# Kernel optimization log

Measured on AMD Instinct MI355X. Metric: run time of the kernel, lower is better.

The kernel has to match this reference:

```python
import jax, jax.numpy as jnp
import numpy as np

N, C, T, V = 32, 256, 256, 25
CI = C // 2
BN_EPS = 1e-5


def setup_inputs() -> dict:
    key = jax.random.key(0)
    ks = jax.random.split(key, 11)
    s = 1.0 / np.sqrt(C)
    si = 1.0 / np.sqrt(CI)
    return {
        "x": jax.random.normal(ks[0], (N, C, T, V), dtype=jnp.float32),
        "Wg": jax.random.normal(ks[1], (CI, C), dtype=jnp.float32) * s,
        "bg": jax.random.normal(ks[2], (CI,), dtype=jnp.float32) * s,
        "Wth": jax.random.normal(ks[3], (CI, C), dtype=jnp.float32) * s,
        "bth": jax.random.normal(ks[4], (CI,), dtype=jnp.float32) * s,
        "Wph": jax.random.normal(ks[5], (CI, C), dtype=jnp.float32) * s,
        "bph": jax.random.normal(ks[6], (CI,), dtype=jnp.float32) * s,
        "Ww": jax.random.normal(ks[7], (C, CI), dtype=jnp.float32) * si,
        "bw": jax.random.normal(ks[8], (C,), dtype=jnp.float32) * si,
        "gamma": jax.random.normal(ks[9], (C,), dtype=jnp.float32) * 0.1,
        "beta": jax.random.normal(ks[10], (C,), dtype=jnp.float32) * 0.1,
    }


def reference(x, Wg, bg, Wth, bth, Wph, bph, Ww, bw, gamma, beta):
    n, c, t, v = x.shape
    ci = Wg.shape[0]
    # [N,C,T,V] -> [N*V, C, T] (permute(0,3,1,2).reshape)
    xf = jnp.transpose(x, (0, 3, 1, 2)).reshape(n * v, c, t)
    # 1x1 Conv1d == channel GEMM
    g_x = jnp.einsum('bct,oc->bot', xf, Wg) + bg[:, None]      # [N*V, Ci, T]
    g_x = g_x.reshape(n, v * ci, t).transpose(0, 2, 1)         # [N, T, V*Ci]
    xmean = xf.reshape(n, v, c, t).mean(axis=1)                # [N, C, T]
    theta = (jnp.einsum('nct,oc->not', xmean, Wth) + bth[:, None]).transpose(0, 2, 1)  # [N,T,Ci]
    phi = jnp.einsum('nct,oc->not', xmean, Wph) + bph[:, None]  # [N, Ci, T]
    f = jnp.matmul(theta, phi)                                  # [N, T, T]
    f = jax.nn.softmax(f, axis=-1)
    y = jnp.matmul(f, g_x)                                      # [N, T, V*Ci]
    y = y.transpose(0, 2, 1).reshape(n * v, ci, t)              # [N*V, Ci, T]
    wy = jnp.einsum('bct,oc->bot', y, Ww) + bw[:, None]         # [N*V, C, T]
    # BatchNorm1d (training mode: batch stats over (batch, T))
    mu = wy.mean(axis=(0, 2))
    var = wy.var(axis=(0, 2))
    wy = (wy - mu[:, None]) * jax.lax.rsqrt(var[:, None] + BN_EPS) * gamma[:, None] + beta[:, None]
    z = wy + xf                                                 # residual
    return jnp.transpose(z.reshape(n, v, c, t), (0, 2, 3, 1))   # [N, C, T, V]
```

## Files before the change

kernel.cpp:

```cpp
#include <hip/hip_runtime.h>

typedef unsigned short u16;
using s8v = __attribute__((ext_vector_type(8))) short;
using f4v = __attribute__((ext_vector_type(4))) float;

constexpr int kN = 32, kC = 256, kT = 256, kV = 25, kCI = 128;
constexpr int kTV = kT * kV;
constexpr int kCIV = kCI * kV;
constexpr int kSAMP = kN * kT * kV;
constexpr int SYY_B = 256;

__device__ __forceinline__ float bf2f(u16 v) {
  return __uint_as_float(((unsigned)v) << 16);
}
__device__ __forceinline__ u16 f2bf(float f) {
  unsigned u = __float_as_uint(f);
  return (u16)((u + 0x7FFFu + ((u >> 16) & 1u)) >> 16);
}

__global__ __launch_bounds__(256) void k_prep(const float* __restrict__ x, u16* __restrict__ x_bf,
                                              float* __restrict__ xm) {
  __shared__ float sm[6400];
  size_t base = (size_t)blockIdx.x * 6400;
  const float4* src = (const float4*)(x + base);
  ushort4* dst = (ushort4*)(x_bf + base);
  for (int i = threadIdx.x; i < 1600; i += 256) {
    float4 v = src[i];
    ((float4*)sm)[i] = v;
    ushort4 b;
    b.x = f2bf(v.x); b.y = f2bf(v.y); b.z = f2bf(v.z); b.w = f2bf(v.w);
    dst[i] = b;
  }
  __syncthreads();
  const float* r = sm + threadIdx.x * 25;
  float s = 0.f;
#pragma unroll
  for (int j = 0; j < 25; ++j) s += r[j];
  xm[(size_t)blockIdx.x * 256 + threadIdx.x] = s * (1.0f / kV);
}

__global__ __launch_bounds__(256) void k_thetaphi(
    const float* __restrict__ xmean, const float* __restrict__ Wth, const float* __restrict__ bth,
    const float* __restrict__ Wph, const float* __restrict__ bph,
    u16* __restrict__ thT, u16* __restrict__ phT) {
  int n = blockIdx.x >> 5;
  int o0 = (blockIdx.x & 31) * 4;
  int t = threadIdx.x;
  __shared__ float wt[4][kC], wp[4][kC];
  for (int i = threadIdx.x; i < 1024; i += 256) {
    wt[i >> 8][i & 255] = Wth[(o0 + (i >> 8)) * kC + (i & 255)];
    wp[i >> 8][i & 255] = Wph[(o0 + (i >> 8)) * kC + (i & 255)];
  }
  __syncthreads();
  const float* xmp = xmean + (size_t)n * kC * kT + t;
  float a[4], p[4];
#pragma unroll
  for (int j = 0; j < 4; ++j) { a[j] = bth[o0 + j]; p[j] = bph[o0 + j]; }
#pragma unroll 4
  for (int c = 0; c < kC; ++c) {
    float xv = xmp[c * kT];
#pragma unroll
    for (int j = 0; j < 4; ++j) {
      a[j] = fmaf(wt[j][c], xv, a[j]);
      p[j] = fmaf(wp[j][c], xv, p[j]);
    }
  }
  size_t rowb = ((size_t)n * kT + t) * kCI + o0;
#pragma unroll
  for (int j = 0; j < 4; ++j) {
    thT[rowb + j] = f2bf(a[j]);
    phT[rowb + j] = f2bf(p[j]);
  }
}

__global__ __launch_bounds__(512) void k_fmfma(const u16* __restrict__ thT, const u16* __restrict__ phT,
                                               u16* __restrict__ f) {
  const int n = blockIdx.x >> 1;
  const int tc0 = (blockIdx.x & 1) * 128;
  const int tid = threadIdx.x, lane = tid & 63, w = tid >> 6;
  const int wM = w & 3, wr = wM * 64, wc = (w >> 2) * 64;
  const int l15 = lane & 15, l4 = lane >> 4;
  __shared__ float redm[4][128], reds[4][128];
  f4v acc[4][4];
#pragma unroll
  for (int i = 0; i < 4; ++i)
#pragma unroll
    for (int j = 0; j < 4; ++j) acc[i][j] = f4v{0.f, 0.f, 0.f, 0.f};
#pragma unroll
  for (int ks = 0; ks < 4; ++ks) {
    s8v af[4], bf[4];
#pragma unroll
    for (int fi = 0; fi < 4; ++fi)
      af[fi] = *(const s8v*)(phT + ((size_t)(n * 256 + wr + fi * 16 + l15) * kCI + ks * 32 + l4 * 8));
#pragma unroll
    for (int g = 0; g < 4; ++g)
      bf[g] = *(const s8v*)(thT + ((size_t)(n * 256 + tc0 + wc + g * 16 + l15) * kCI + ks * 32 + l4 * 8));
#pragma unroll
    for (int g = 0; g < 4; ++g)
#pragma unroll
      for (int fi = 0; fi < 4; ++fi)
        acc[fi][g] = __builtin_amdgcn_mfma_f32_16x16x32_bf16(af[fi], bf[g], acc[fi][g], 0, 0, 0);
  }
  float mx[4], sm[4];
#pragma unroll
  for (int g = 0; g < 4; ++g) {
    float m = -1e30f;
#pragma unroll
    for (int fi = 0; fi < 4; ++fi)
#pragma unroll
      for (int r = 0; r < 4; ++r) m = fmaxf(m, acc[fi][g][r]);
    m = fmaxf(m, __shfl_xor(m, 16));
    m = fmaxf(m, __shfl_xor(m, 32));
    mx[g] = m;
  }
  if (l4 == 0)
#pragma unroll
    for (int g = 0; g < 4; ++g) redm[wM][wc + g * 16 + l15] = mx[g];
  __syncthreads();
#pragma unroll
  for (int g = 0; g < 4; ++g) {
    int col = wc + g * 16 + l15;
    mx[g] = fmaxf(fmaxf(redm[0][col], redm[1][col]), fmaxf(redm[2][col], redm[3][col]));
  }
#pragma unroll
  for (int g = 0; g < 4; ++g) {
    float s = 0.f;
#pragma unroll
    for (int fi = 0; fi < 4; ++fi)
#pragma unroll
      for (int r = 0; r < 4; ++r) {
        float e = __expf(acc[fi][g][r] - mx[g]);
        acc[fi][g][r] = e;
        s += e;
      }
    s += __shfl_xor(s, 16);
    s += __shfl_xor(s, 32);
    sm[g] = s;
  }
  if (l4 == 0)
#pragma unroll
    for (int g = 0; g < 4; ++g) reds[wM][wc + g * 16 + l15] = sm[g];
  __syncthreads();
#pragma unroll
  for (int g = 0; g < 4; ++g) {
    int col = wc + g * 16 + l15;
    float inv = 1.0f / (reds[0][col] + reds[1][col] + reds[2][col] + reds[3][col]);
    int t = tc0 + col;
#pragma unroll
    for (int fi = 0; fi < 4; ++fi) {
      int tp0 = wr + fi * 16 + l4 * 4;
      ushort4 st;
      st.x = f2bf(acc[fi][g][0] * inv);
      st.y = f2bf(acc[fi][g][1] * inv);
      st.z = f2bf(acc[fi][g][2] * inv);
      st.w = f2bf(acc[fi][g][3] * inv);
      *(ushort4*)(f + (size_t)(n * 256 + t) * 256 + tp0) = st;
    }
  }
}

__global__ __launch_bounds__(256) void k_cvtW(const float* __restrict__ Wg, const float* __restrict__ Ww,
                                              u16* __restrict__ Wg_fl, u16* __restrict__ Ww_fl) {
  int i = blockIdx.x * 256 + threadIdx.x;
  { int m = i >> 8, k = i & 255; Wg_fl[(size_t)((k >> 3) * 128 + m) * 8 + (k & 7)] = f2bf(Wg[i]); }
  { int m = i >> 7, k = i & 127; Ww_fl[(size_t)((k >> 3) * 256 + m) * 8 + (k & 7)] = f2bf(Ww[i]); }
}

template <int K_TOT, int NCOLS, int MODE>
__global__ __launch_bounds__(256) void k_gemm(
    const u16* __restrict__ A_, const u16* __restrict__ B_, const float* __restrict__ bias,
    void* __restrict__ outp, const float* __restrict__ scale, const float* __restrict__ shift,
    const u16* __restrict__ xres) {
  constexpr int KSTEPS = K_TOT / 32;
  constexpr int M_TOT = (MODE == 0) ? 128 : 256;
  __shared__ uint4 Bs[512];
  const int n = blockIdx.z, m0 = blockIdx.y * 128, n0 = blockIdx.x * 128;
  const int tid = threadIdx.x, lane = tid & 63, w = tid >> 6;
  const int wr = (w >> 1) * 64, wc = (w & 1) * 64;
  const int l15 = lane & 15, l4 = lane >> 4;
  const u16* Bn = B_ + (size_t)n * K_TOT * NCOLS + n0;
  const int scol = tid & 127, sk0 = tid >> 7;
  f4v acc[4][4];
#pragma unroll
  for (int i = 0; i < 4; ++i)
#pragma unroll
    for (int j = 0; j < 4; ++j) acc[i][j] = f4v{0.f, 0.f, 0.f, 0.f};

  for (int ks = 0; ks < KSTEPS; ++ks) {
    __syncthreads();
#pragma unroll
    for (int p = 0; p < 2; ++p) {
      int ksub = sk0 + p * 2;
      const u16* src = Bn + (size_t)(ks * 32 + ksub * 8) * NCOLS + scol;
      union { u16 u[8]; uint4 v; } pk;
#pragma unroll
      for (int j = 0; j < 8; ++j) pk.u[j] = src[(size_t)j * NCOLS];
      int blk = ksub * 128 + scol;
      blk ^= (blk >> 2) & 3;
      Bs[blk] = pk.v;
    }
    __syncthreads();
    s8v af[4];
#pragma unroll
    for (int fi = 0; fi < 4; ++fi) {
      int m = m0 + wr + fi * 16 + l15;
      const u16* ap;
      if constexpr (MODE == 1)
        ap = A_ + ((size_t)(n * 256 + m) * 256 + ks * 32 + l4 * 8);
      else
        ap = A_ + (size_t)((ks * 4 + l4) * M_TOT + m) * 8;
      af[fi] = *(const s8v*)ap;
    }
#pragma unroll
    for (int g = 0; g < 4; ++g) {
      int blk = l4 * 128 + wc + g * 16 + l15;
      blk ^= (blk >> 2) & 3;
      s8v bf = *(const s8v*)&Bs[blk];
#pragma unroll
      for (int fi = 0; fi < 4; ++fi)
        acc[fi][g] = __builtin_amdgcn_mfma_f32_16x16x32_bf16(af[fi], bf, acc[fi][g], 0, 0, 0);
    }
  }
#pragma unroll
  for (int fi = 0; fi < 4; ++fi) {
    int growb = m0 + wr + fi * 16 + l4 * 4;
#pragma unroll
    for (int g = 0; g < 4; ++g) {
      int gcol = n0 + wc + g * 16 + l15;
#pragma unroll
      for (int r = 0; r < 4; ++r) {
        int grow = growb + r;
        float vv = acc[fi][g][r];
        if constexpr (MODE == 0) {
          vv += bias[grow];
          int t = gcol / 25, v5 = gcol - t * 25;
          ((u16*)outp)[((size_t)n * kT + t) * kCIV + grow * 25 + v5] = f2bf(vv);
        } else if constexpr (MODE == 1) {
          int ci = gcol / 25, v5 = gcol - ci * 25;
          ((u16*)outp)[((size_t)n * kCI + ci) * kTV + grow * 25 + v5] = f2bf(vv);
        } else {
          size_t idx = ((size_t)n * kC + grow) * kTV + gcol;
          ((float*)outp)[idx] = vv * scale[grow] + shift[grow] + bf2f(xres[idx]);
        }
      }
    }
  }
}

__global__ __launch_bounds__(256) void k_syy(const u16* __restrict__ yb, float* __restrict__ psyy,
                                             float* __restrict__ psy) {
  const int b = blockIdx.x, n = b >> 3, kc = b & 7;
  const int kbase = kc * 800;
  const int tid = threadIdx.x, lane = tid & 63, w = tid >> 6;
  const int wr = (w >> 1) * 64, wc = (w & 1) * 64, l15 = lane & 15, l4 = lane >> 4;
  const u16* Y = yb + (size_t)n * kCI * kTV;
  f4v acc[4][4];
#pragma unroll
  for (int i = 0; i < 4; ++i)
#pragma unroll
    for (int j = 0; j < 4; ++j) acc[i][j] = f4v{0.f, 0.f, 0.f, 0.f};
  float syl[4] = {0.f, 0.f, 0.f, 0.f};
  for (int ks = 0; ks < 25; ++ks) {
    int k = kbase + ks * 32 + l4 * 8;
    s8v af[4], bf[4];
#pragma unroll
    for (int fi = 0; fi < 4; ++fi) {
      af[fi] = *(const s8v*)(Y + (size_t)(wr + fi * 16 + l15) * kTV + k);
      bf[fi] = *(const s8v*)(Y + (size_t)(wc + fi * 16 + l15) * kTV + k);
    }
#pragma unroll
    for (int fi = 0; fi < 4; ++fi)
#pragma unroll
      for (int j = 0; j < 8; ++j) syl[fi] += bf2f((u16)af[fi][j]);
#pragma unroll
    for (int g = 0; g < 4; ++g)
#pragma unroll
      for (int fi = 0; fi < 4; ++fi)
        acc[fi][g] = __builtin_amdgcn_mfma_f32_16x16x32_bf16(af[fi], bf[g], acc[fi][g], 0, 0, 0);
  }
  float* pb = psyy + (size_t)b * 16384;
#pragma unroll
  for (int fi = 0; fi < 4; ++fi)
#pragma unroll
    for (int g = 0; g < 4; ++g)
#pragma unroll
      for (int r = 0; r < 4; ++r)
        pb[(wr + fi * 16 + l4 * 4 + r) * kCI + wc + g * 16 + l15] = acc[fi][g][r];
#pragma unroll
  for (int fi = 0; fi < 4; ++fi) {
    float s = syl[fi];
    s += __shfl_xor(s, 16);
    s += __shfl_xor(s, 32);
    if ((w & 1) == 0 && l4 == 0) psy[b * kCI + wr + fi * 16 + l15] = s;
  }
}

__global__ __launch_bounds__(256) void k_reduce(const float* __restrict__ psyy, const float* __restrict__ psy,
                                                float* __restrict__ syy, float* __restrict__ sy) {
  if (blockIdx.x < 64) {
    int i = blockIdx.x * 256 + threadIdx.x;
    float s = 0.f;
    for (int b = 0; b < SYY_B; ++b) s += psyy[(size_t)b * 16384 + i];
    syy[i] = s;
  } else if (threadIdx.x < kCI) {
    float s = 0.f;
    for (int b = 0; b < SYY_B; ++b) s += psy[b * kCI + threadIdx.x];
    sy[threadIdx.x] = s;
  }
}

__global__ __launch_bounds__(128) void k_stats(const float* __restrict__ syy, const float* __restrict__ sy,
                                               const float* __restrict__ Ww, const float* __restrict__ bw,
                                               const float* __restrict__ gamma, const float* __restrict__ beta,
                                               float* __restrict__ scale, float* __restrict__ shift) {
  int c2 = blockIdx.x;
  int tid = threadIdx.x;
  __shared__ float wsm[kCI];
  __shared__ float red1[kCI], red2[kCI];
  wsm[tid] = Ww[c2 * kCI + tid];
  __syncthreads();
  float val = 0.f;
#pragma unroll 8
  for (int ci = 0; ci < kCI; ++ci) val = fmaf(wsm[ci], syy[ci * kCI + tid], val);
  red1[tid] = wsm[tid] * sy[tid];
  red2[tid] = val * wsm[tid];
  __syncthreads();
  for (int s = 64; s > 0; s >>= 1) {
    if (tid < s) { red1[tid] += red1[tid + s]; red2[tid] += red2[tid + s]; }
    __syncthreads();
  }
  if (tid == 0) {
    const float invS = 1.0f / (float)kSAMP;
    float m1 = red1[0] * invS;
    float b = bw[c2];
    float mu = m1 + b;
    float e2 = red2[0] * invS + 2.f * b * m1 + b * b;
    float var = e2 - mu * mu;
    float rstd = rsqrtf(var + 1e-5f);
    float sc = rstd * gamma[c2];
    scale[c2] = sc;
    shift[c2] = beta[c2] + (b - mu) * sc;
  }
}

extern "C" void kernel_launch(void* const* d_in, const int* in_sizes, int n_in,
                              void* d_out, int out_size, void* d_ws, size_t ws_size,
                              hipStream_t stream) {
  const float* x     = (const float*)d_in[0];
  const float* Wg    = (const float*)d_in[1];
  const float* bg    = (const float*)d_in[2];
  const float* Wth   = (const float*)d_in[3];
  const float* bth   = (const float*)d_in[4];
  const float* Wph   = (const float*)d_in[5];
  const float* bph   = (const float*)d_in[6];
  const float* Ww    = (const float*)d_in[7];
  const float* bw    = (const float*)d_in[8];
  const float* gamma = (const float*)d_in[9];
  const float* beta  = (const float*)d_in[10];
  float* out = (float*)d_out;

  char* wsb = (char*)d_ws;
  float* xmean = (float*)(wsb);
  u16*   thT   = (u16*)(wsb + (8u << 20));
  u16*   phT   = (u16*)(wsb + (10u << 20));
  u16*   f_bf  = (u16*)(wsb + (12u << 20));
  float* psy   = (float*)(wsb + (16u << 20));
  float* syy   = (float*)(wsb + (17u << 20));
  float* sy    = syy + 16384;
  float* scale = sy + 128;
  float* shift = scale + 256;
  u16* Wg_fl = (u16*)(wsb + (18u << 20));
  u16* Ww_fl = Wg_fl + 32768;
  u16* x_bf  = (u16*)(wsb + (19u << 20));
  u16* g2    = (u16*)(wsb + (119u << 20));
  float* psyy = (float*)(wsb + (119u << 20));
  u16* yb    = (u16*)(wsb + (172u << 20));

  k_prep<<<8192, 256, 0, stream>>>(x, x_bf, xmean);
  k_cvtW<<<128, 256, 0, stream>>>(Wg, Ww, Wg_fl, Ww_fl);
  k_thetaphi<<<1024, 256, 0, stream>>>(xmean, Wth, bth, Wph, bph, thT, phT);
  k_fmfma<<<64, 512, 0, stream>>>(thT, phT, f_bf);
  k_gemm<256, kTV, 0><<<dim3(50, 1, 32), 256, 0, stream>>>(
      Wg_fl, x_bf, bg, (void*)g2, nullptr, nullptr, nullptr);
  k_gemm<256, kCIV, 1><<<dim3(25, 2, 32), 256, 0, stream>>>(
      f_bf, g2, nullptr, (void*)yb, nullptr, nullptr, nullptr);
  k_syy<<<SYY_B, 256, 0, stream>>>(yb, psyy, psy);
  k_reduce<<<65, 256, 0, stream>>>(psyy, psy, syy, sy);
  k_stats<<<256, 128, 0, stream>>>(syy, sy, Ww, bw, gamma, beta, scale, shift);
  k_gemm<128, kTV, 2><<<dim3(50, 2, 32), 256, 0, stream>>>(
      Ww_fl, yb, nullptr, (void*)out, scale, shift, x_bf);
}
```

Measured before the change: 363.5 us.

## Store GEMM operands in k-packed fragment layout and drop LDS staging

Producers (k_prep, k_fmfma, the g and y GEMM epilogues) now write their bf16 outputs in a layout that packs 8 consecutive k values per column. This lets k_gemm load A and B MFMA fragments directly from global memory as 16-byte vectors, removing the strided scalar gathers, LDS staging and barriers. The y GEMM writes both a row-major copy for the stats kernel and a packed copy for the final GEMM. The residual now reads the fp32 input x directly instead of a bf16 copy. The cost is extra write traffic and possible cache pressure from relying on global memory for fragment reuse.

Result: slower. 450.2 us (+23.9%).

```diff
diff --git a/kernel.cpp b/kernel.cpp
--- a/kernel.cpp
+++ b/kernel.cpp
@@ -6,7 +6,6 @@
 
 constexpr int kN = 32, kC = 256, kT = 256, kV = 25, kCI = 128;
 constexpr int kTV = kT * kV;
-constexpr int kCIV = kCI * kV;
 constexpr int kSAMP = kN * kT * kV;
 constexpr int SYY_B = 256;
 
@@ -18,25 +17,36 @@
   return (u16)((u + 0x7FFFu + ((u >> 16) & 1u)) >> 16);
 }
 
-__global__ __launch_bounds__(256) void k_prep(const float* __restrict__ x, u16* __restrict__ x_bf,
+__global__ __launch_bounds__(256) void k_prep(const float* __restrict__ x, u16* __restrict__ x_fl,
                                               float* __restrict__ xm) {
-  __shared__ float sm[6400];
-  size_t base = (size_t)blockIdx.x * 6400;
-  const float4* src = (const float4*)(x + base);
-  ushort4* dst = (ushort4*)(x_bf + base);
-  for (int i = threadIdx.x; i < 1600; i += 256) {
-    float4 v = src[i];
-    ((float4*)sm)[i] = v;
-    ushort4 b;
-    b.x = f2bf(v.x); b.y = f2bf(v.y); b.z = f2bf(v.z); b.w = f2bf(v.w);
-    dst[i] = b;
-  }
-  __syncthreads();
-  const float* r = sm + threadIdx.x * 25;
-  float s = 0.f;
-#pragma unroll
-  for (int j = 0; j < 25; ++j) s += r[j];
-  xm[(size_t)blockIdx.x * 256 + threadIdx.x] = s * (1.0f / kV);
+  __shared__ float sm[8][1600];
+  const int n = blockIdx.x >> 5, cg = blockIdx.x & 31;
+  const int tid = threadIdx.x;
+  u16* xfn = x_fl + (size_t)n * (kC / 8) * kTV * 8;
+  for (int chunk = 0; chunk < 4; ++chunk) {
+    const int col0 = chunk * 1600;
+    for (int e = tid; e < 3200; e += 256) {
+      int r = e / 400, c4 = e % 400;
+      float4 v = *(const float4*)(x + ((size_t)(n * kC + cg * 8 + r) * kTV + col0) + c4 * 4);
+      *(float4*)&sm[r][c4 * 4] = v;
+    }
+    __syncthreads();
+    for (int col = tid; col < 1600; col += 256) {
+      union { u16 u[8]; uint4 v; } pk;
+#pragma unroll
+      for (int r = 0; r < 8; ++r) pk.u[r] = f2bf(sm[r][col]);
+      *(uint4*)(xfn + (size_t)(cg * kTV + col0 + col) * 8) = pk.v;
+    }
+    for (int i = tid; i < 512; i += 256) {
+      int c = i >> 6, tl = i & 63;
+      float s = 0.f;
+      const float* p = &sm[c][tl * 25];
+#pragma unroll
+      for (int j = 0; j < 25; ++j) s += p[j];
+      xm[(size_t)(n * kC + cg * 8 + c) * kT + chunk * 64 + tl] = s * (1.0f / kV);
+    }
+    __syncthreads();
+  }
 }
 
 __global__ __launch_bounds__(256) void k_thetaphi(
@@ -74,7 +84,7 @@
 }
 
 __global__ __launch_bounds__(512) void k_fmfma(const u16* __restrict__ thT, const u16* __restrict__ phT,
-                                               u16* __restrict__ f) {
+                                               u16* __restrict__ f_fl) {
   const int n = blockIdx.x >> 1;
   const int tc0 = (blockIdx.x & 1) * 128;
   const int tid = threadIdx.x, lane = tid & 63, w = tid >> 6;
@@ -154,7 +164,7 @@
       st.y = f2bf(acc[fi][g][1] * inv);
       st.z = f2bf(acc[fi][g][2] * inv);
       st.w = f2bf(acc[fi][g][3] * inv);
-      *(ushort4*)(f + (size_t)(n * 256 + t) * 256 + tp0) = st;
+      *(ushort4*)(f_fl + (size_t)n * 65536 + (size_t)((tp0 >> 3) * 256 + t) * 8 + (tp0 & 7)) = st;
     }
   }
 }
@@ -169,57 +179,37 @@
 template <int K_TOT, int NCOLS, int MODE>
 __global__ __launch_bounds__(256) void k_gemm(
     const u16* __restrict__ A_, const u16* __restrict__ B_, const float* __restrict__ bias,
-    void* __restrict__ outp, const float* __restrict__ scale, const float* __restrict__ shift,
-    const u16* __restrict__ xres) {
+    void* __restrict__ outp, void* __restrict__ outp2, const float* __restrict__ scale,
+    const float* __restrict__ shift, const float* __restrict__ xres) {
   constexpr int KSTEPS = K_TOT / 32;
   constexpr int M_TOT = (MODE == 0) ? 128 : 256;
-  __shared__ uint4 Bs[512];
   const int n = blockIdx.z, m0 = blockIdx.y * 128, n0 = blockIdx.x * 128;
   const int tid = threadIdx.x, lane = tid & 63, w = tid >> 6;
   const int wr = (w >> 1) * 64, wc = (w & 1) * 64;
   const int l15 = lane & 15, l4 = lane >> 4;
-  const u16* Bn = B_ + (size_t)n * K_TOT * NCOLS + n0;
-  const int scol = tid & 127, sk0 = tid >> 7;
+  const u16* Bn = B_ + (size_t)n * (K_TOT / 8) * NCOLS * 8;
+  const u16* An = (MODE == 1) ? A_ + (size_t)n * 65536 : A_;
   f4v acc[4][4];
 #pragma unroll
   for (int i = 0; i < 4; ++i)
 #pragma unroll
     for (int j = 0; j < 4; ++j) acc[i][j] = f4v{0.f, 0.f, 0.f, 0.f};
 
+#pragma unroll 2
   for (int ks = 0; ks < KSTEPS; ++ks) {
-    __syncthreads();
-#pragma unroll
-    for (int p = 0; p < 2; ++p) {
-      int ksub = sk0 + p * 2;
-      const u16* src = Bn + (size_t)(ks * 32 + ksub * 8) * NCOLS + scol;
-      union { u16 u[8]; uint4 v; } pk;
-#pragma unroll
-      for (int j = 0; j < 8; ++j) pk.u[j] = src[(size_t)j * NCOLS];
-      int blk = ksub * 128 + scol;
-      blk ^= (blk >> 2) & 3;
-      Bs[blk] = pk.v;
-    }
-    __syncthreads();
-    s8v af[4];
-#pragma unroll
-    for (int fi = 0; fi < 4; ++fi) {
-      int m = m0 + wr + fi * 16 + l15;
-      const u16* ap;
-      if constexpr (MODE == 1)
-        ap = A_ + ((size_t)(n * 256 + m) * 256 + ks * 32 + l4 * 8);
-      else
-        ap = A_ + (size_t)((ks * 4 + l4) * M_TOT + m) * 8;
-      af[fi] = *(const s8v*)ap;
-    }
-#pragma unroll
-    for (int g = 0; g < 4; ++g) {
-      int blk = l4 * 128 + wc + g * 16 + l15;
-      blk ^= (blk >> 2) & 3;
-      s8v bf = *(const s8v*)&Bs[blk];
+    const int ksub = ks * 4 + l4;
+    s8v af[4], bf[4];
+#pragma unroll
+    for (int fi = 0; fi < 4; ++fi)
+      af[fi] = *(const s8v*)(An + (size_t)(ksub * M_TOT + m0 + wr + fi * 16 + l15) * 8);
+#pragma unroll
+    for (int g = 0; g < 4; ++g)
+      bf[g] = *(const s8v*)(Bn + (size_t)(ksub * NCOLS + n0 + wc + g * 16 + l15) * 8);
+#pragma unroll
+    for (int g = 0; g < 4; ++g)
 #pragma unroll
       for (int fi = 0; fi < 4; ++fi)
-        acc[fi][g] = __builtin_amdgcn_mfma_f32_16x16x32_bf16(af[fi], bf, acc[fi][g], 0, 0, 0);
-    }
+        acc[fi][g] = __builtin_amdgcn_mfma_f32_16x16x32_bf16(af[fi], bf[g], acc[fi][g], 0, 0, 0);
   }
 #pragma unroll
   for (int fi = 0; fi < 4; ++fi) {
@@ -234,13 +224,15 @@
         if constexpr (MODE == 0) {
           vv += bias[grow];
           int t = gcol / 25, v5 = gcol - t * 25;
-          ((u16*)outp)[((size_t)n * kT + t) * kCIV + grow * 25 + v5] = f2bf(vv);
+          ((u16*)outp)[(size_t)n * 819200 + (size_t)((t >> 3) * 3200 + grow * 25 + v5) * 8 + (t & 7)] = f2bf(vv);
         } else if constexpr (MODE == 1) {
           int ci = gcol / 25, v5 = gcol - ci * 25;
-          ((u16*)outp)[((size_t)n * kCI + ci) * kTV + grow * 25 + v5] = f2bf(vv);
+          u16 b = f2bf(vv);
+          ((u16*)outp)[((size_t)n * kCI + ci) * kTV + grow * 25 + v5] = b;
+          ((u16*)outp2)[(size_t)n * 819200 + (size_t)((ci >> 3) * 6400 + grow * 25 + v5) * 8 + (ci & 7)] = b;
         } else {
           size_t idx = ((size_t)n * kC + grow) * kTV + gcol;
-          ((float*)outp)[idx] = vv * scale[grow] + shift[grow] + bf2f(xres[idx]);
+          ((float*)outp)[idx] = vv * scale[grow] + shift[grow] + xres[idx];
         }
       }
     }
@@ -363,7 +355,7 @@
   float* xmean = (float*)(wsb);
   u16*   thT   = (u16*)(wsb + (8u << 20));
   u16*   phT   = (u16*)(wsb + (10u << 20));
-  u16*   f_bf  = (u16*)(wsb + (12u << 20));
+  u16*   f_fl  = (u16*)(wsb + (12u << 20));
   float* psy   = (float*)(wsb + (16u << 20));
   float* syy   = (float*)(wsb + (17u << 20));
   float* sy    = syy + 16384;
@@ -371,22 +363,23 @@
   float* shift = scale + 256;
   u16* Wg_fl = (u16*)(wsb + (18u << 20));
   u16* Ww_fl = Wg_fl + 32768;
-  u16* x_bf  = (u16*)(wsb + (19u << 20));
-  u16* g2    = (u16*)(wsb + (119u << 20));
+  u16* x_fl  = (u16*)(wsb + (19u << 20));
+  u16* yb_fl = x_fl;
+  u16* g2_fl = (u16*)(wsb + (119u << 20));
   float* psyy = (float*)(wsb + (119u << 20));
-  u16* yb    = (u16*)(wsb + (172u << 20));
-
-  k_prep<<<8192, 256, 0, stream>>>(x, x_bf, xmean);
+  u16* yb_rm = (u16*)(wsb + (169u << 20));
+
+  k_prep<<<1024, 256, 0, stream>>>(x, x_fl, xmean);
   k_cvtW<<<128, 256, 0, stream>>>(Wg, Ww, Wg_fl, Ww_fl);
   k_thetaphi<<<1024, 256, 0, stream>>>(xmean, Wth, bth, Wph, bph, thT, phT);
-  k_fmfma<<<64, 512, 0, stream>>>(thT, phT, f_bf);
+  k_fmfma<<<64, 512, 0, stream>>>(thT, phT, f_fl);
   k_gemm<256, kTV, 0><<<dim3(50, 1, 32), 256, 0, stream>>>(
-      Wg_fl, x_bf, bg, (void*)g2, nullptr, nullptr, nullptr);
-  k_gemm<256, kCIV, 1><<<dim3(25, 2, 32), 256, 0, stream>>>(
-      f_bf, g2, nullptr, (void*)yb, nullptr, nullptr, nullptr);
-  k_syy<<<SYY_B, 256, 0, stream>>>(yb, psyy, psy);
+      Wg_fl, x_fl, bg, (void*)g2_fl, nullptr, nullptr, nullptr, nullptr);
+  k_gemm<256, 3200, 1><<<dim3(25, 2, 32), 256, 0, stream>>>(
+      f_fl, g2_fl, nullptr, (void*)yb_rm, (void*)yb_fl, nullptr, nullptr, nullptr);
+  k_syy<<<SYY_B, 256, 0, stream>>>(yb_rm, psyy, psy);
   k_reduce<<<65, 256, 0, stream>>>(psyy, psy, syy, sy);
   k_stats<<<256, 128, 0, stream>>>(syy, sy, Ww, bw, gamma, beta, scale, shift);
   k_gemm<128, kTV, 2><<<dim3(50, 2, 32), 256, 0, stream>>>(
-      Ww_fl, yb, nullptr, (void*)out, scale, shift, x_bf);
-}
+      Ww_fl, yb_fl, nullptr, (void*)out, nullptr, scale, shift, x);
+}
```

## Fuse theta/phi projection into attention kernel using MFMA on bf16 weights

Applied to the files above, without the earlier changes.

Removes the scalar FP32 theta/phi projection kernel and instead computes theta and phi inside the attention kernel with bf16 MFMA, staging xmean as bf16 in LDS and keeping the projected values in LDS for the T×T score GEMM and softmax. Wth and Wph are converted to a fragment-friendly bf16 layout in the weight conversion kernel. This drops one launch and the global round trip of theta/phi. In exchange, each of the 64 blocks recomputes phi for all 256 time steps, xmean is now rounded to bf16 before the projection, and the fused kernel uses large LDS with only 64 blocks running.

New measurement: 354.0 us. 2.6% less time.

```diff
diff --git a/kernel.cpp b/kernel.cpp
--- a/kernel.cpp
+++ b/kernel.cpp
@@ -39,68 +39,111 @@
   xm[(size_t)blockIdx.x * 256 + threadIdx.x] = s * (1.0f / kV);
 }
 
-__global__ __launch_bounds__(256) void k_thetaphi(
-    const float* __restrict__ xmean, const float* __restrict__ Wth, const float* __restrict__ bth,
-    const float* __restrict__ Wph, const float* __restrict__ bph,
-    u16* __restrict__ thT, u16* __restrict__ phT) {
-  int n = blockIdx.x >> 5;
-  int o0 = (blockIdx.x & 31) * 4;
-  int t = threadIdx.x;
-  __shared__ float wt[4][kC], wp[4][kC];
-  for (int i = threadIdx.x; i < 1024; i += 256) {
-    wt[i >> 8][i & 255] = Wth[(o0 + (i >> 8)) * kC + (i & 255)];
-    wp[i >> 8][i & 255] = Wph[(o0 + (i >> 8)) * kC + (i & 255)];
-  }
-  __syncthreads();
-  const float* xmp = xmean + (size_t)n * kC * kT + t;
-  float a[4], p[4];
-#pragma unroll
-  for (int j = 0; j < 4; ++j) { a[j] = bth[o0 + j]; p[j] = bph[o0 + j]; }
-#pragma unroll 4
-  for (int c = 0; c < kC; ++c) {
-    float xv = xmp[c * kT];
-#pragma unroll
-    for (int j = 0; j < 4; ++j) {
-      a[j] = fmaf(wt[j][c], xv, a[j]);
-      p[j] = fmaf(wp[j][c], xv, p[j]);
-    }
-  }
-  size_t rowb = ((size_t)n * kT + t) * kCI + o0;
-#pragma unroll
-  for (int j = 0; j < 4; ++j) {
-    thT[rowb + j] = f2bf(a[j]);
-    phT[rowb + j] = f2bf(p[j]);
-  }
-}
-
-__global__ __launch_bounds__(512) void k_fmfma(const u16* __restrict__ thT, const u16* __restrict__ phT,
+__global__ __launch_bounds__(256) void k_cvtW(const float* __restrict__ Wg, const float* __restrict__ Ww,
+                                              const float* __restrict__ Wth, const float* __restrict__ Wph,
+                                              u16* __restrict__ Wg_fl, u16* __restrict__ Ww_fl,
+                                              u16* __restrict__ Wthph_fl) {
+  int i = blockIdx.x * 256 + threadIdx.x;
+  { int m = i >> 8, k = i & 255; Wg_fl[(size_t)((k >> 3) * 128 + m) * 8 + (k & 7)] = f2bf(Wg[i]); }
+  { int m = i >> 7, k = i & 127; Ww_fl[(size_t)((k >> 3) * 256 + m) * 8 + (k & 7)] = f2bf(Ww[i]); }
+  { int m = i >> 8, k = i & 255;
+    Wthph_fl[(size_t)((k >> 3) * 256 + m) * 8 + (k & 7)] = f2bf(Wth[i]);
+    Wthph_fl[(size_t)((k >> 3) * 256 + (m + 128)) * 8 + (k & 7)] = f2bf(Wph[i]); }
+}
+
+__global__ __launch_bounds__(512) void k_fattn(const float* __restrict__ xmean,
+                                               const u16* __restrict__ Wthph_fl,
+                                               const float* __restrict__ bth, const float* __restrict__ bph,
                                                u16* __restrict__ f) {
-  const int n = blockIdx.x >> 1;
-  const int tc0 = (blockIdx.x & 1) * 128;
+  __shared__ __align__(16) u16 lds[49152];
+  const int n = blockIdx.x >> 1, tc0 = (blockIdx.x & 1) * 128;
   const int tid = threadIdx.x, lane = tid & 63, w = tid >> 6;
-  const int wM = w & 3, wr = wM * 64, wc = (w >> 2) * 64;
   const int l15 = lane & 15, l4 = lane >> 4;
-  __shared__ float redm[4][128], reds[4][128];
-  f4v acc[4][4];
+  const int wro = (w & 3) * 64, wct = (w >> 2) * 128;
+  f4v acc[4][8];
 #pragma unroll
   for (int i = 0; i < 4; ++i)
 #pragma unroll
-    for (int j = 0; j < 4; ++j) acc[i][j] = f4v{0.f, 0.f, 0.f, 0.f};
+    for (int j = 0; j < 8; ++j) acc[i][j] = f4v{0.f, 0.f, 0.f, 0.f};
+  for (int ch = 0; ch < 2; ++ch) {
+    __syncthreads();
+    for (int e = tid; e < 8192; e += 512) {
+      int cc = e >> 6, t4 = (e & 63) * 4;
+      float4 v = *(const float4*)(xmean + (((size_t)(n * 256 + ch * 128 + cc)) << 8) + t4);
+      u16* d = &lds[(((cc >> 3) * 256 + t4) << 3) + (cc & 7)];
+      d[0] = f2bf(v.x); d[8] = f2bf(v.y); d[16] = f2bf(v.z); d[24] = f2bf(v.w);
+    }
+    __syncthreads();
+#pragma unroll
+    for (int ks = 0; ks < 4; ++ks) {
+      const int ksub = ks * 4 + l4;
+      s8v af[4], bf[8];
+#pragma unroll
+      for (int fi = 0; fi < 4; ++fi)
+        af[fi] = *(const s8v*)(Wthph_fl + (size_t)((ch * 16 + ksub) * 256 + wro + fi * 16 + l15) * 8);
+#pragma unroll
+      for (int g = 0; g < 8; ++g)
+        bf[g] = *(const s8v*)&lds[((ksub * 256 + wct + g * 16 + l15) << 3)];
+#pragma unroll
+      for (int g = 0; g < 8; ++g)
+#pragma unroll
+        for (int fi = 0; fi < 4; ++fi)
+          acc[fi][g] = __builtin_amdgcn_mfma_f32_16x16x32_bf16(af[fi], bf[g], acc[fi][g], 0, 0, 0);
+    }
+  }
+  __syncthreads();
+#pragma unroll
+  for (int fi = 0; fi < 4; ++fi) {
+    int o0 = wro + fi * 16 + l4 * 4;
+    bool isTh = o0 < 128;
+    float bb[4];
+#pragma unroll
+    for (int r = 0; r < 4; ++r) bb[r] = isTh ? bth[o0 + r] : bph[o0 - 128 + r];
+#pragma unroll
+    for (int g = 0; g < 8; ++g) {
+      int t = wct + g * 16 + l15;
+      ushort4 pk;
+      pk.x = f2bf(acc[fi][g][0] + bb[0]);
+      pk.y = f2bf(acc[fi][g][1] + bb[1]);
+      pk.z = f2bf(acc[fi][g][2] + bb[2]);
+      pk.w = f2bf(acc[fi][g][3] + bb[3]);
+      if (isTh) {
+        unsigned tl = (unsigned)(t - tc0);
+        if (tl < 128u)
+          *(ushort4*)&lds[(((o0 >> 3) * 128 + (int)tl) << 3) + (o0 & 7)] = pk;
+      } else {
+        int o = o0 - 128;
+        *(ushort4*)&lds[16384 + (((o >> 3) * 256 + t) << 3) + (o & 7)] = pk;
+      }
+    }
+  }
+  __syncthreads();
+  const int wr = (w & 3) * 64, wcc = (w >> 2) * 64;
+  const int wM = w & 3;
+  f4v facc[4][4];
+#pragma unroll
+  for (int i = 0; i < 4; ++i)
+#pragma unroll
+    for (int j = 0; j < 4; ++j) facc[i][j] = f4v{0.f, 0.f, 0.f, 0.f};
 #pragma unroll
   for (int ks = 0; ks < 4; ++ks) {
+    const int ksub = ks * 4 + l4;
     s8v af[4], bf[4];
 #pragma unroll
     for (int fi = 0; fi < 4; ++fi)
-      af[fi] = *(const s8v*)(phT + ((size_t)(n * 256 + wr + fi * 16 + l15) * kCI + ks * 32 + l4 * 8));
+      af[fi] = *(const s8v*)&lds[16384 + ((ksub * 256 + wr + fi * 16 + l15) << 3)];
 #pragma unroll
     for (int g = 0; g < 4; ++g)
-      bf[g] = *(const s8v*)(thT + ((size_t)(n * 256 + tc0 + wc + g * 16 + l15) * kCI + ks * 32 + l4 * 8));
+      bf[g] = *(const s8v*)&lds[((ksub * 128 + wcc + g * 16 + l15) << 3)];
 #pragma unroll
     for (int g = 0; g < 4; ++g)
 #pragma unroll
       for (int fi = 0; fi < 4; ++fi)
-        acc[fi][g] = __builtin_amdgcn_mfma_f32_16x16x32_bf16(af[fi], bf[g], acc[fi][g], 0, 0, 0);
-  }
+        facc[fi][g] = __builtin_amdgcn_mfma_f32_16x16x32_bf16(af[fi], bf[g], facc[fi][g], 0, 0, 0);
+  }
+  __syncthreads();
+  float* redm = (float*)lds;
+  float* reds = redm + 512;
   float mx[4], sm[4];
 #pragma unroll
   for (int g = 0; g < 4; ++g) {
@@ -108,19 +151,19 @@
 #pragma unroll
     for (int fi = 0; fi < 4; ++fi)
 #pragma unroll
-      for (int r = 0; r < 4; ++r) m = fmaxf(m, acc[fi][g][r]);
+      for (int r = 0; r < 4; ++r) m = fmaxf(m, facc[fi][g][r]);
     m = fmaxf(m, __shfl_xor(m, 16));
     m = fmaxf(m, __shfl_xor(m, 32));
     mx[g] = m;
   }
   if (l4 == 0)
 #pragma unroll
-    for (int g = 0; g < 4; ++g) redm[wM][wc + g * 16 + l15] = mx[g];
+    for (int g = 0; g < 4; ++g) redm[wM * 128 + wcc + g * 16 + l15] = mx[g];
   __syncthreads();
 #pragma unroll
   for (int g = 0; g < 4; ++g) {
-    int col = wc + g * 16 + l15;
-    mx[g] = fmaxf(fmaxf(redm[0][col], redm[1][col]), fmaxf(redm[2][col], redm[3][col]));
+    int col = wcc + g * 16 + l15;
+    mx[g] = fmaxf(fmaxf(redm[col], redm[128 + col]), fmaxf(redm[256 + col], redm[384 + col]));
   }
 #pragma unroll
   for (int g = 0; g < 4; ++g) {
@@ -129,8 +172,8 @@
     for (int fi = 0; fi < 4; ++fi)
 #pragma unroll
       for (int r = 0; r < 4; ++r) {
-        float e = __expf(acc[fi][g][r] - mx[g]);
-        acc[fi][g][r] = e;
+        float e = __expf(facc[fi][g][r] - mx[g]);
+        facc[fi][g][r] = e;
         s += e;
       }
     s += __shfl_xor(s, 16);
@@ -139,31 +182,24 @@
   }
   if (l4 == 0)
 #pragma unroll
-    for (int g = 0; g < 4; ++g) reds[wM][wc + g * 16 + l15] = sm[g];
+    for (int g = 0; g < 4; ++g) reds[wM * 128 + wcc + g * 16 + l15] = sm[g];
   __syncthreads();
 #pragma unroll
   for (int g = 0; g < 4; ++g) {
-    int col = wc + g * 16 + l15;
-    float inv = 1.0f / (reds[0][col] + reds[1][col] + reds[2][col] + reds[3][col]);
+    int col = wcc + g * 16 + l15;
+    float inv = 1.0f / (reds[col] + reds[128 + col] + reds[256 + col] + reds[384 + col]);
     int t = tc0 + col;
 #pragma unroll
     for (int fi = 0; fi < 4; ++fi) {
       int tp0 = wr + fi * 16 + l4 * 4;
       ushort4 st;
-      st.x = f2bf(acc[fi][g][0] * inv);
-      st.y = f2bf(acc[fi][g][1] * inv);
-      st.z = f2bf(acc[fi][g][2] * inv);
-      st.w = f2bf(acc[fi][g][3] * inv);
+      st.x = f2bf(facc[fi][g][0] * inv);
+      st.y = f2bf(facc[fi][g][1] * inv);
+      st.z = f2bf(facc[fi][g][2] * inv);
+      st.w = f2bf(facc[fi][g][3] * inv);
       *(ushort4*)(f + (size_t)(n * 256 + t) * 256 + tp0) = st;
     }
   }
-}
-
-__global__ __launch_bounds__(256) void k_cvtW(const float* __restrict__ Wg, const float* __restrict__ Ww,
-                                              u16* __restrict__ Wg_fl, u16* __restrict__ Ww_fl) {
-  int i = blockIdx.x * 256 + threadIdx.x;
-  { int m = i >> 8, k = i & 255; Wg_fl[(size_t)((k >> 3) * 128 + m) * 8 + (k & 7)] = f2bf(Wg[i]); }
-  { int m = i >> 7, k = i & 127; Ww_fl[(size_t)((k >> 3) * 256 + m) * 8 + (k & 7)] = f2bf(Ww[i]); }
 }
 
 template <int K_TOT, int NCOLS, int MODE>
@@ -361,8 +397,7 @@
 
   char* wsb = (char*)d_ws;
   float* xmean = (float*)(wsb);
-  u16*   thT   = (u16*)(wsb + (8u << 20));
-  u16*   phT   = (u16*)(wsb + (10u << 20));
+  u16* Wthph_fl = (u16*)(wsb + (8u << 20));
   u16*   f_bf  = (u16*)(wsb + (12u << 20));
   float* psy   = (float*)(wsb + (16u << 20));
   float* syy   = (float*)(wsb + (17u << 20));
@@ -376,10 +411,9 @@
   float* psyy = (float*)(wsb + (119u << 20));
   u16* yb    = (u16*)(wsb + (172u << 20));
 
+  k_cvtW<<<128, 256, 0, stream>>>(Wg, Ww, Wth, Wph, Wg_fl, Ww_fl, Wthph_fl);
   k_prep<<<8192, 256, 0, stream>>>(x, x_bf, xmean);
-  k_cvtW<<<128, 256, 0, stream>>>(Wg, Ww, Wg_fl, Ww_fl);
-  k_thetaphi<<<1024, 256, 0, stream>>>(xmean, Wth, bth, Wph, bph, thT, phT);
-  k_fmfma<<<64, 512, 0, stream>>>(thT, phT, f_bf);
+  k_fattn<<<64, 512, 0, stream>>>(xmean, Wthph_fl, bth, bph, f_bf);
   k_gemm<256, kTV, 0><<<dim3(50, 1, 32), 256, 0, stream>>>(
       Wg_fl, x_bf, bg, (void*)g2, nullptr, nullptr, nullptr);
   k_gemm<256, kCIV, 1><<<dim3(25, 2, 32), 256, 0, stream>>>(
```
